# Kernel tuning notes

Measured on AMD Instinct MI355X. Metric: run time of the kernel, lower is better.

## Reference

```python
import jax, jax.numpy as jnp
import numpy as np

H, I, B, S = 3200, 12800, 8, 1024  # InternViT-6B MLP dims


def setup_inputs() -> dict:
    key = jax.random.key(0)
    ks = jax.random.split(key, 8)
    # int8-valued activations/weights stored as int32 (harness dtype set)
    hidden_states = jax.random.randint(ks[0], (B, S, H), -127, 128, dtype=jnp.int32)
    scale = jax.random.uniform(ks[1], (B * S,), dtype=jnp.float32) * 1e-3 + 1e-5
    w1 = jax.random.randint(ks[2], (I, H), -127, 128, dtype=jnp.int32)
    w1_scale = jax.random.uniform(ks[3], (I,), dtype=jnp.float32) * 1e-3 + 1e-5
    b1 = jax.random.normal(ks[4], (I,), dtype=jnp.float32) * 0.02
    w2 = jax.random.randint(ks[5], (H, I), -127, 128, dtype=jnp.int32)
    w2_scale = jax.random.uniform(ks[6], (H,), dtype=jnp.float32) * 1e-3 + 1e-5
    b2 = jax.random.normal(ks[7], (H,), dtype=jnp.float32) * 0.02
    return {"hidden_states": hidden_states, "scale": scale, "w1": w1,
            "w1_scale": w1_scale, "b1": b1, "w2": w2, "w2_scale": w2_scale, "b2": b2}


def _w8a8_linear(x_q, x_scale, w_q, w_scale, b):
    # enough that fp32 matmul reproduces the exact integer accumulator to
    # within float32 rounding of the final sum.
    acc = jnp.matmul(x_q.astype(jnp.float32), w_q.astype(jnp.float32).T)  # [T, out]
    out = acc * x_scale[:, None] * w_scale[None, :] + b[None, :]
    return out.astype(jnp.float16)


def reference(hidden_states, scale, w1, w1_scale, b1, w2, w2_scale, b2):
    bsz, seq, hidden = hidden_states.shape
    x_q = hidden_states.reshape(-1, hidden)                 # [T, H] int8 values
    # fc1: W8A8 -> fp16 with dynamic per-token input scale
    fc1_out = _w8a8_linear(x_q, scale, w1, w1_scale, b1)    # [T, I] fp16
    # fused gelu_and_quant: exact GELU, then per-token dynamic int8 re-quant
    g = jax.nn.gelu(fc1_out.astype(jnp.float32), approximate=False)  # [T, I]
    new_scale = jnp.max(jnp.abs(g), axis=-1) / 127.0        # dynamic per-token scale
    act_q = jnp.clip(jnp.round(g / new_scale[:, None]), -127, 127)  # int8 values
    # fc2: W8A8 -> fp16
    out = _w8a8_linear(act_q, new_scale, w2, w2_scale, b2)  # [T, H] fp16
    return out
```

## Files before the change

kernel.cpp:

```cpp
#include <hip/hip_runtime.h>
#include <hip/hip_bf16.h>
#include <hip/hip_fp16.h>

#define T_DIM 8192
#define H_DIM 3200
#define I_DIM 12800

typedef int v4i __attribute__((ext_vector_type(4)));
typedef _Float16 h8 __attribute__((ext_vector_type(8)));

__device__ __forceinline__ void gload16(const void* g, void* l) {
    __builtin_amdgcn_global_load_lds(
        (const __attribute__((address_space(1))) unsigned int*)g,
        (__attribute__((address_space(3))) unsigned int*)l, 16, 0, 0);
}

__global__ __launch_bounds__(256) void repack_kernel(const int* __restrict__ src,
                                                     unsigned int* __restrict__ dst,
                                                     long n4) {
    long i = (long)blockIdx.x * blockDim.x + threadIdx.x;
    long stride = (long)gridDim.x * blockDim.x;
    for (; i < n4; i += stride) {
        int4 v = ((const int4*)src)[i];
        dst[i] = (unsigned int)((v.x & 255) | ((v.y & 255) << 8) |
                                ((v.z & 255) << 16) | ((v.w & 255) << 24));
    }
}

template <int EPI>
__global__ __launch_bounds__(512, 2) void gemm_i8_8ph(
    const signed char* __restrict__ A, long strideA,
    const signed char* __restrict__ B, long strideB,
    int Ntrue, int K, int ldc,
    const float* __restrict__ rowscale, const float* __restrict__ colscale,
    const float* __restrict__ bias, void* __restrict__ Cout) {
    __shared__ signed char lds[131072];
    signed char* ldsA = lds;
    signed char* ldsB = lds + 65536;

    const int tid = threadIdx.x;
    const int lane = tid & 63, wid = tid >> 6;
    const int wr = wid >> 2, wc = wid & 3;
    const int bm = blockIdx.x, bn = blockIdx.y;
    const long Arow0 = (long)bm * 256;
    const long Bcol0 = (long)bn * 256;

    const int c0 = tid, c1 = tid + 512;
    const int r0 = c0 >> 2, r1 = c1 >> 2;
    const int s0 = (((c0 & 3) ^ ((r0 >> 1) & 3)) << 4);
    const int s1 = (((c1 & 3) ^ ((r1 >> 1) & 3)) << 4);
    const signed char* Ag0 = A + (Arow0 + r0) * strideA + s0;
    const signed char* Ag1 = A + (Arow0 + r1) * strideA + s1;
    const signed char* Bg0 = B + (Bcol0 + r0) * strideB + s0;
    const signed char* Bg1 = B + (Bcol0 + r1) * strideB + s1;
    const int d0 = c0 * 16, d1 = c1 * 16;

    const int NH = K >> 6;
    const int nkt = K >> 7;

#define STAGE_A(h)                                  \
    {                                               \
        const int hc_ = (h) < NH ? (h) : NH - 1;    \
        const long ko_ = (long)hc_ << 6;            \
        signed char* d_ = ldsA + (((h) & 3) << 14); \
        gload16(Ag0 + ko_, d_ + d0);                \
        gload16(Ag1 + ko_, d_ + d1);                \
    }
#define STAGE_B(h)                                  \
    {                                               \
        const int hc_ = (h) < NH ? (h) : NH - 1;    \
        const long ko_ = (long)hc_ << 6;            \
        signed char* d_ = ldsB + (((h) & 3) << 14); \
        gload16(Bg0 + ko_, d_ + d0);                \
        gload16(Bg1 + ko_, d_ + d1);                \
    }

    const int r = lane & 15, q = lane >> 4;
    const int swz = ((q ^ ((r >> 1) & 3)) << 4);
    const int aoff = (wr * 128 + r) * 64 + swz;
    const int boff = (wc * 64 + r) * 64 + swz;

    v4i acc[8][4] = {};
    v4i af[4], bf[4];

#define PHASE(SLOTA, SLOTB, AIDX, LOADB, ACCOFF, STAGE_STMT, GATE_STMT)     \
    {                                                                       \
        _Pragma("unroll") for (int i = 0; i < 4; ++i)                       \
            af[i] = *(const v4i*)((SLOTA) + aoff + ((AIDX) + i) * 1024);    \
        if (LOADB) {                                                        \
            _Pragma("unroll") for (int n = 0; n < 4; ++n)                   \
                bf[n] = *(const v4i*)((SLOTB) + boff + n * 1024);           \
        }                                                                   \
        STAGE_STMT;                                                         \
        __builtin_amdgcn_s_setprio(1);                                      \
        _Pragma("unroll") for (int m = 0; m < 4; ++m)                       \
            _Pragma("unroll") for (int n = 0; n < 4; ++n)                   \
                acc[m + (ACCOFF)][n] = __builtin_amdgcn_mfma_i32_16x16x64_i8( \
                    af[m], bf[n], acc[m + (ACCOFF)][n], 0, 0, 0);           \
        __builtin_amdgcn_s_setprio(0);                                      \
        GATE_STMT;                                                          \
        __builtin_amdgcn_s_barrier();                                       \
    }

    STAGE_B(0); STAGE_A(0); STAGE_B(1); STAGE_A(1);
    STAGE_B(2); STAGE_A(2); STAGE_B(3);
    asm volatile("s_waitcnt vmcnt(6)");
    __builtin_amdgcn_s_barrier();

    for (int kt = 0; kt < nkt; ++kt) {
        const int g = kt << 1;
        const signed char* sA0 = ldsA + ((g & 3) << 14);
        const signed char* sB0 = ldsB + ((g & 3) << 14);
        const signed char* sA1 = ldsA + (((g + 1) & 3) << 14);
        const signed char* sB1 = ldsB + (((g + 1) & 3) << 14);
        PHASE(sA0, sB0, 0, true, 0, STAGE_A(g + 3), );
        PHASE(sA0, sB0, 4, false, 4, STAGE_B(g + 4), );
        PHASE(sA1, sB1, 0, true, 0, STAGE_A(g + 4), );
        PHASE(sA1, sB1, 4, false, 4, STAGE_B(g + 5),
              asm volatile("s_waitcnt vmcnt(6)"));
    }

    const int row0 = bm * 256 + wr * 128;
    const int col0 = bn * 256 + wc * 64;
    const int r4 = (lane >> 4) << 2, cl = lane & 15;
#pragma unroll
    for (int m = 0; m < 8; ++m) {
        const int rowb = row0 + m * 16 + r4;
        float rs[4];
#pragma unroll
        for (int rr = 0; rr < 4; ++rr) rs[rr] = rowscale[rowb + rr];
#pragma unroll
        for (int n = 0; n < 4; ++n) {
            const int col = col0 + n * 16 + cl;
            if (col < Ntrue) {
                const float cs = colscale[col];
                const float bs = bias[col];
#pragma unroll
                for (int rr = 0; rr < 4; ++rr) {
                    float v = (float)acc[m][n][rr];
                    v = __fmul_rn(v, rs[rr]);
                    v = __fmul_rn(v, cs);
                    v = __fadd_rn(v, bs);
                    _Float16 hh = (_Float16)v;
                    const size_t idx = (size_t)(rowb + rr) * ldc + col;
                    if (EPI == 0) ((_Float16*)Cout)[idx] = hh;
                    else ((float*)Cout)[idx] = (float)hh;
                }
            }
        }
    }
#undef PHASE
#undef STAGE_A
#undef STAGE_B
}

__global__ __launch_bounds__(256) void gelu_quant(_Float16* __restrict__ fc1,
                                                  float* __restrict__ nscale) {
    __shared__ float gbuf[I_DIM];
    __shared__ float wmax[4];
    const int tid = threadIdx.x, lane = tid & 63, wid = tid >> 6;
    const long t = blockIdx.x;
    const h8* row = (const h8*)(fc1 + t * I_DIM);
    float lmax = 0.f;
    for (int c = tid; c < I_DIM / 8; c += 256) {
        h8 v = row[c];
#pragma unroll
        for (int j = 0; j < 8; ++j) {
            float x = (float)v[j];
            float e = erff(__fdiv_rn(x, 1.41421356237309504880f));
            float g = __fmul_rn(__fmul_rn(0.5f, x), __fadd_rn(1.0f, e));
            gbuf[c * 8 + j] = g;
            lmax = fmaxf(lmax, fabsf(g));
        }
    }
#pragma unroll
    for (int off = 32; off; off >>= 1) lmax = fmaxf(lmax, __shfl_xor(lmax, off, 64));
    if (lane == 0) wmax[wid] = lmax;
    __syncthreads();
    const float gmax = fmaxf(fmaxf(wmax[0], wmax[1]), fmaxf(wmax[2], wmax[3]));
    const float ns = gmax / 127.0f;
    if (tid == 0) nscale[t] = ns;
    unsigned long long* out = (unsigned long long*)(fc1 + t * I_DIM);
    for (int c = tid; c < I_DIM / 8; c += 256) {
        unsigned long long pk = 0;
#pragma unroll
        for (int j = 0; j < 8; ++j) {
            float qv = rintf(__fdiv_rn(gbuf[c * 8 + j], ns));
            qv = fminf(fmaxf(qv, -127.f), 127.f);
            pk |= ((unsigned long long)(unsigned char)(signed char)(int)qv) << (8 * j);
        }
        out[c] = pk;
    }
}

extern "C" void kernel_launch(void* const* d_in, const int* in_sizes, int n_in,
                              void* d_out, int out_size, void* d_ws, size_t ws_size,
                              hipStream_t stream) {
    const int* hs = (const int*)d_in[0];
    const float* scale = (const float*)d_in[1];
    const int* w1 = (const int*)d_in[2];
    const float* w1s = (const float*)d_in[3];
    const float* b1 = (const float*)d_in[4];
    const int* w2 = (const int*)d_in[5];
    const float* w2s = (const float*)d_in[6];
    const float* b2 = (const float*)d_in[7];

    char* ws = (char*)d_ws;
    signed char* xq = (signed char*)ws;
    signed char* w1q = xq + (size_t)T_DIM * H_DIM;
    signed char* w2q = w1q + (size_t)I_DIM * H_DIM;
    _Float16* fc1h = (_Float16*)(w2q + (size_t)H_DIM * I_DIM);
    const size_t fixed = (size_t)T_DIM * H_DIM + 2 * (size_t)I_DIM * H_DIM;

    int nc = 1;
    while (nc < 16) {
        size_t need = fixed + ((size_t)T_DIM / nc) * I_DIM * 2 +
                      ((size_t)T_DIM / nc) * 4 + 256;
        if (need <= ws_size) break;
        nc <<= 1;
    }
    const int chunkT = T_DIM / nc;
    float* nscale = (float*)((char*)fc1h + (size_t)chunkT * I_DIM * 2);

    repack_kernel<<<2048, 256, 0, stream>>>(hs, (unsigned int*)xq, (long)T_DIM * H_DIM / 4);
    repack_kernel<<<2048, 256, 0, stream>>>(w1, (unsigned int*)w1q, (long)I_DIM * H_DIM / 4);
    repack_kernel<<<2048, 256, 0, stream>>>(w2, (unsigned int*)w2q, (long)H_DIM * I_DIM / 4);

    const int n2tiles = (H_DIM + 255) / 256;
    for (int c = 0; c < nc; ++c) {
        const int t0 = c * chunkT;
        gemm_i8_8ph<0><<<dim3(chunkT / 256, I_DIM / 256), 512, 0, stream>>>(
            xq + (size_t)t0 * H_DIM, (long)H_DIM, w1q, (long)H_DIM,
            I_DIM, H_DIM, I_DIM,
            scale + t0, w1s, b1, (void*)fc1h);
        gelu_quant<<<chunkT, 256, 0, stream>>>(fc1h, nscale);
        gemm_i8_8ph<1><<<dim3(chunkT / 256, n2tiles), 512, 0, stream>>>(
            (const signed char*)fc1h, (long)I_DIM * 2, w2q, (long)I_DIM,
            H_DIM, I_DIM, H_DIM,
            nscale, w2s, b2,
            (void*)((float*)d_out + (size_t)t0 * H_DIM));
    }
}
```

Baseline: 950.9 us.

## Split GEMM block into 16 waves with 64x64 per-wave tiles

```diff
diff --git a/kernel.cpp b/kernel.cpp
--- a/kernel.cpp
+++ b/kernel.cpp
@@ -28,7 +28,7 @@
 }
 
 template <int EPI>
-__global__ __launch_bounds__(512, 2) void gemm_i8_8ph(
+__global__ __launch_bounds__(1024, 4) void gemm_i8_16w(
     const signed char* __restrict__ A, long strideA,
     const signed char* __restrict__ B, long strideB,
     int Ntrue, int K, int ldc,
@@ -45,86 +45,60 @@
     const long Arow0 = (long)bm * 256;
     const long Bcol0 = (long)bn * 256;
 
-    const int c0 = tid, c1 = tid + 512;
-    const int r0 = c0 >> 2, r1 = c1 >> 2;
-    const int s0 = (((c0 & 3) ^ ((r0 >> 1) & 3)) << 4);
-    const int s1 = (((c1 & 3) ^ ((r1 >> 1) & 3)) << 4);
+    const int r0 = tid >> 2;
+    const int s0 = (((tid & 3) ^ ((r0 >> 1) & 3)) << 4);
     const signed char* Ag0 = A + (Arow0 + r0) * strideA + s0;
-    const signed char* Ag1 = A + (Arow0 + r1) * strideA + s1;
     const signed char* Bg0 = B + (Bcol0 + r0) * strideB + s0;
-    const signed char* Bg1 = B + (Bcol0 + r1) * strideB + s1;
-    const int d0 = c0 * 16, d1 = c1 * 16;
+    const int d0 = tid * 16;
 
     const int NH = K >> 6;
-    const int nkt = K >> 7;
-
-#define STAGE_A(h)                                  \
+
+#define STAGE_AB(h)                                 \
     {                                               \
         const int hc_ = (h) < NH ? (h) : NH - 1;    \
         const long ko_ = (long)hc_ << 6;            \
-        signed char* d_ = ldsA + (((h) & 3) << 14); \
-        gload16(Ag0 + ko_, d_ + d0);                \
-        gload16(Ag1 + ko_, d_ + d1);                \
-    }
-#define STAGE_B(h)                                  \
-    {                                               \
-        const int hc_ = (h) < NH ? (h) : NH - 1;    \
-        const long ko_ = (long)hc_ << 6;            \
-        signed char* d_ = ldsB + (((h) & 3) << 14); \
-        gload16(Bg0 + ko_, d_ + d0);                \
-        gload16(Bg1 + ko_, d_ + d1);                \
+        const int sl_ = ((h) & 3) << 14;            \
+        gload16(Ag0 + ko_, ldsA + sl_ + d0);        \
+        gload16(Bg0 + ko_, ldsB + sl_ + d0);        \
     }
 
     const int r = lane & 15, q = lane >> 4;
     const int swz = ((q ^ ((r >> 1) & 3)) << 4);
-    const int aoff = (wr * 128 + r) * 64 + swz;
+    const int aoff = (wr * 64 + r) * 64 + swz;
     const int boff = (wc * 64 + r) * 64 + swz;
 
-    v4i acc[8][4] = {};
+    v4i acc[4][4] = {};
     v4i af[4], bf[4];
 
-#define PHASE(SLOTA, SLOTB, AIDX, LOADB, ACCOFF, STAGE_STMT, GATE_STMT)     \
-    {                                                                       \
-        _Pragma("unroll") for (int i = 0; i < 4; ++i)                       \
-            af[i] = *(const v4i*)((SLOTA) + aoff + ((AIDX) + i) * 1024);    \
-        if (LOADB) {                                                        \
-            _Pragma("unroll") for (int n = 0; n < 4; ++n)                   \
-                bf[n] = *(const v4i*)((SLOTB) + boff + n * 1024);           \
-        }                                                                   \
-        STAGE_STMT;                                                         \
-        __builtin_amdgcn_s_setprio(1);                                      \
-        _Pragma("unroll") for (int m = 0; m < 4; ++m)                       \
-            _Pragma("unroll") for (int n = 0; n < 4; ++n)                   \
-                acc[m + (ACCOFF)][n] = __builtin_amdgcn_mfma_i32_16x16x64_i8( \
-                    af[m], bf[n], acc[m + (ACCOFF)][n], 0, 0, 0);           \
-        __builtin_amdgcn_s_setprio(0);                                      \
-        GATE_STMT;                                                          \
-        __builtin_amdgcn_s_barrier();                                       \
-    }
-
-    STAGE_B(0); STAGE_A(0); STAGE_B(1); STAGE_A(1);
-    STAGE_B(2); STAGE_A(2); STAGE_B(3);
-    asm volatile("s_waitcnt vmcnt(6)");
+    STAGE_AB(0); STAGE_AB(1); STAGE_AB(2);
+    asm volatile("s_waitcnt vmcnt(4)");
     __builtin_amdgcn_s_barrier();
 
-    for (int kt = 0; kt < nkt; ++kt) {
-        const int g = kt << 1;
-        const signed char* sA0 = ldsA + ((g & 3) << 14);
-        const signed char* sB0 = ldsB + ((g & 3) << 14);
-        const signed char* sA1 = ldsA + (((g + 1) & 3) << 14);
-        const signed char* sB1 = ldsB + (((g + 1) & 3) << 14);
-        PHASE(sA0, sB0, 0, true, 0, STAGE_A(g + 3), );
-        PHASE(sA0, sB0, 4, false, 4, STAGE_B(g + 4), );
-        PHASE(sA1, sB1, 0, true, 0, STAGE_A(g + 4), );
-        PHASE(sA1, sB1, 4, false, 4, STAGE_B(g + 5),
-              asm volatile("s_waitcnt vmcnt(6)"));
-    }
-
-    const int row0 = bm * 256 + wr * 128;
+    for (int h = 0; h < NH; ++h) {
+        const signed char* sA = ldsA + ((h & 3) << 14);
+        const signed char* sB = ldsB + ((h & 3) << 14);
+#pragma unroll
+        for (int i = 0; i < 4; ++i) af[i] = *(const v4i*)(sA + aoff + i * 1024);
+#pragma unroll
+        for (int n = 0; n < 4; ++n) bf[n] = *(const v4i*)(sB + boff + n * 1024);
+        STAGE_AB(h + 3);
+        __builtin_amdgcn_s_setprio(1);
+#pragma unroll
+        for (int m = 0; m < 4; ++m)
+#pragma unroll
+            for (int n = 0; n < 4; ++n)
+                acc[m][n] = __builtin_amdgcn_mfma_i32_16x16x64_i8(
+                    af[m], bf[n], acc[m][n], 0, 0, 0);
+        __builtin_amdgcn_s_setprio(0);
+        asm volatile("s_waitcnt vmcnt(4)");
+        __builtin_amdgcn_s_barrier();
+    }
+
+    const int row0 = bm * 256 + wr * 64;
     const int col0 = bn * 256 + wc * 64;
     const int r4 = (lane >> 4) << 2, cl = lane & 15;
 #pragma unroll
-    for (int m = 0; m < 8; ++m) {
+    for (int m = 0; m < 4; ++m) {
         const int rowb = row0 + m * 16 + r4;
         float rs[4];
 #pragma unroll
@@ -149,9 +123,7 @@
             }
         }
     }
-#undef PHASE
-#undef STAGE_A
-#undef STAGE_B
+#undef STAGE_AB
 }
 
 __global__ __launch_bounds__(256) void gelu_quant(_Float16* __restrict__ fc1,
@@ -229,12 +201,12 @@
     const int n2tiles = (H_DIM + 255) / 256;
     for (int c = 0; c < nc; ++c) {
         const int t0 = c * chunkT;
-        gemm_i8_8ph<0><<<dim3(chunkT / 256, I_DIM / 256), 512, 0, stream>>>(
+        gemm_i8_16w<0><<<dim3(chunkT / 256, I_DIM / 256), 1024, 0, stream>>>(
             xq + (size_t)t0 * H_DIM, (long)H_DIM, w1q, (long)H_DIM,
             I_DIM, H_DIM, I_DIM,
             scale + t0, w1s, b1, (void*)fc1h);
         gelu_quant<<<chunkT, 256, 0, stream>>>(fc1h, nscale);
-        gemm_i8_8ph<1><<<dim3(chunkT / 256, n2tiles), 512, 0, stream>>>(
+        gemm_i8_16w<1><<<dim3(chunkT / 256, n2tiles), 1024, 0, stream>>>(
             (const signed char*)fc1h, (long)I_DIM * 2, w2q, (long)I_DIM,
             H_DIM, I_DIM, H_DIM,
             nscale, w2s, b2,
```

Measured after the change: 949.1 us (median of 2 runs). No clear change (-0.2%).
